# Performance work log

Hardware: AMD Instinct MI355X
Metric: run time of the kernel (lower is better)

## Reference

```python
import jax, jax.numpy as jnp
import numpy as np

Q_MIN = 0.01
PT_THLD = 0.9
MAX_ETA = 4.0
LW_REP = 1.0
LW_NOISE = 0.1
LW_COWARD = 0.1
EPS = 1e-9

N_HITS = 50000
N_CLUSTERS = 1024  # cluster id 0 = noise, ids 1..K-1 = objects
D_EMB = 32


def setup_inputs() -> dict:
    key = jax.random.key(0)
    k0, k1, k2, k3, k4, k5 = jax.random.split(key, 6)
    beta = jax.random.uniform(k0, (N_HITS,), dtype=jnp.float32)
    x = jax.random.normal(k1, (N_HITS, D_EMB), dtype=jnp.float32)
    pt = jax.random.uniform(k2, (N_HITS,), dtype=jnp.float32)
    eta = jax.random.normal(k3, (N_HITS,), dtype=jnp.float32)
    reconstructable = jax.random.randint(k4, (N_HITS,), 0, 2, dtype=jnp.int32)
    cluster_ids = jax.random.randint(k5, (N_HITS,), 0, N_CLUSTERS, dtype=jnp.int64)
    return {
        'beta': beta, 'x': x, 'pt': pt, 'eta': eta,
        'reconstructable': reconstructable, 'cluster_ids': cluster_ids,
        'n_clusters': N_CLUSTERS,
    }


def reference(beta, x, pt, eta, reconstructable, cluster_ids, n_clusters):
    K = int(n_clusters)
    n_hits = beta.shape[0]
    n_part = K - 1  # objects of interest (excluding noise id 0)

    # charge q_j = arctanh(beta)^2 + q_min
    q = jnp.arctanh(jnp.clip(beta, 0.0, 1.0 - 1e-4)) ** 2 + Q_MIN  # [N]

    # attractive membership mask [N, K-1]: hit j belongs to object k and passes filters
    oids = jnp.arange(1, K)
    hit_ok = (reconstructable > 0) & (pt > PT_THLD) & (jnp.abs(eta) < MAX_ETA)
    att = (cluster_ids[:, None] == oids[None, :]) & hit_ok[:, None]
    attf = att.astype(q.dtype)

    # condensation point per object: hit with max charge within the object
    alphas = jnp.argmax(q[:, None] * attf, axis=0)  # [K-1]
    q_k = q[alphas]
    x_k = x[alphas]  # [K-1, D]

    # pairwise Euclidean distances, GEMM form (avoids [N,K,D] intermediate)
    d2 = (jnp.sum(x * x, axis=1)[:, None]
          + jnp.sum(x_k * x_k, axis=1)[None, :]
          - 2.0 * (x @ x_k.T))
    dist = jnp.sqrt(jnp.maximum(d2, 1e-12))  # [N, K-1]

    qw = q[:, None] * q_k[None, :]

    n_hits_oi = jnp.sum(hit_ok).astype(q.dtype)
    norm_att = EPS + n_hits_oi - n_part
    norm_rep = EPS + (n_part - 1) * n_hits

    v_att = jnp.sum(qw * (dist ** 2) * attf) / norm_att

    rep = (~att) & (dist < 1.0)  # max_n_rep=0 -> no subsampling
    v_rep = jnp.sum(qw * (1.0 - dist) * rep.astype(q.dtype)) / norm_rep

    l_coward = jnp.mean(1.0 - beta[alphas])

    noise_mask = (cluster_ids <= 0).astype(q.dtype)  # noise_threshold = 0
    l_noise = jnp.sum(beta * noise_mask) / jnp.maximum(jnp.sum(noise_mask), 1.0)

    total = v_att + LW_REP * v_rep + LW_NOISE * l_noise + LW_COWARD * l_coward
    return total
```

## Files before the change

kernel.cpp:

```cpp
#include <hip/hip_runtime.h>
#include <math.h>

namespace {

constexpr int D = 32;
constexpr int KOBJ = 1023;
constexpr float QMIN = 0.01f;
constexpr float PTT = 0.9f;
constexpr float METAETA = 4.0f;

typedef __attribute__((ext_vector_type(8))) short short8;
typedef __attribute__((ext_vector_type(4))) float f32x4;

#define GLOAD_LDS16(g, l)                                              \
  __builtin_amdgcn_global_load_lds(                                    \
      (const __attribute__((address_space(1))) void*)(g),              \
      (__attribute__((address_space(3))) void*)(l), 16, 0, 0)

__device__ inline float waveSum(float v) {
#pragma unroll
  for (int o = 32; o > 0; o >>= 1) v += __shfl_down(v, o, 64);
  return v;
}

__device__ inline ushort f2bf(float f) {
  unsigned u = __float_as_uint(f);
  return (ushort)((u + 0x7FFFu + ((u >> 16) & 1u)) >> 16);
}

__global__ void k_init(int* wsbase) {
  int i = blockIdx.x * 256 + threadIdx.x;
  if (i < 2064) wsbase[i] = 0;
}

__global__ __launch_bounds__(256) void k_hits(
    const float* __restrict__ beta, const float* __restrict__ x,
    const float* __restrict__ pt, const float* __restrict__ eta,
    const int* __restrict__ recon, const int* __restrict__ cidw,
    int N, float* acc, unsigned long long* keys,
    float* __restrict__ qArr, float* __restrict__ nxArr,
    int* __restrict__ attkArr) {
  int t = threadIdx.x;
  int j = blockIdx.x * 256 + t;
  int odd = 2 * (t & 127) + 1;
  int ow = (odd < N) ? cidw[odd] : 0;
  int is64 = !__any(ow != 0);
  bool ok = false;
  if (j < N) {
    int cid = is64 ? cidw[2 * j] : cidw[j];
    float b = beta[j];
    float bc = fminf(fmaxf(b, 0.f), 1.f - 1e-4f);
    float tt = atanhf(bc);
    float q = tt * tt + QMIN;
    ok = (recon[j] > 0) && (pt[j] > PTT) && (fabsf(eta[j]) < METAETA);
    float nx = 0.f;
    const float4* xr = (const float4*)(x + (size_t)j * D);
#pragma unroll
    for (int i2 = 0; i2 < 8; ++i2) {
      float4 v = xr[i2];
      nx += v.x * v.x + v.y * v.y + v.z * v.z + v.w * v.w;
    }
    int attk = (ok && cid >= 1) ? cid : 0;
    qArr[j] = q;
    nxArr[j] = nx;
    attkArr[j] = attk;
    if (cid <= 0) {
      atomicAdd(&acc[2], b);
      atomicAdd(&acc[3], 1.f);
    }
    if (attk >= 1) {
      unsigned long long key =
          (((unsigned long long)__float_as_uint(q)) << 32) |
          (unsigned long long)(0xFFFFFFFFu - (unsigned)j);
      atomicMax(&keys[attk - 1], key);
    }
  }
  unsigned long long bal = __ballot(ok);
  if ((t & 63) == 0 && bal)
    atomicAdd(&acc[4], (float)__popcll(bal));
}

__global__ __launch_bounds__(256, 2) void k_clusters(
    const float* __restrict__ beta, const float* __restrict__ x,
    const unsigned long long* __restrict__ keys,
    const float* __restrict__ qArr, const float* __restrict__ nxArr,
    int* __restrict__ alphaArr, float2* __restrict__ qnk,
    ushort* __restrict__ xkbT, float* acc) {
  int k = blockIdx.x * blockDim.x + threadIdx.x;
  float cw = 0.f;
  if (k < KOBJ) {
    unsigned long long key = keys[k];
    int alpha = (key != 0ull) ? (int)(0xFFFFFFFFu - (unsigned)(key & 0xFFFFFFFFull)) : 0;
    alphaArr[k] = alpha;
    qnk[k] = make_float2(qArr[alpha], nxArr[alpha]);
    const float4* s4 = (const float4*)(x + (size_t)alpha * D);
    float4 v[8];
#pragma unroll
    for (int i = 0; i < 8; ++i) v[i] = s4[i];
#pragma unroll
    for (int s = 0; s < 4; ++s) {
      float4 v0 = v[2 * s], v1 = v[2 * s + 1];
      ushort* dst = xkbT + (size_t)s * 8192 + (size_t)k * 8;
      dst[0] = f2bf(v0.x); dst[1] = f2bf(v0.y);
      dst[2] = f2bf(v0.z); dst[3] = f2bf(v0.w);
      dst[4] = f2bf(v1.x); dst[5] = f2bf(v1.y);
      dst[6] = f2bf(v1.z); dst[7] = f2bf(v1.w);
    }
    cw = 1.f - beta[alpha];
  } else if (k == KOBJ) {
    qnk[k] = make_float2(0.f, 1e30f);
#pragma unroll
    for (int s = 0; s < 4; ++s) {
      ushort* dst = xkbT + (size_t)s * 8192 + (size_t)k * 8;
#pragma unroll
      for (int e = 0; e < 8; ++e) dst[e] = 0;
    }
  }
  float s = waveSum(cw);
  if ((threadIdx.x & 63) == 0 && s != 0.f) atomicAdd(&acc[5], s);
}

__global__ __launch_bounds__(256) void k_pair(
    const float* __restrict__ x, int N,
    const float* __restrict__ qArr, const float* __restrict__ nxArr,
    const int* __restrict__ attkArr, const int* __restrict__ alphaArr,
    const float2* __restrict__ qnk, const ushort* __restrict__ xkbT,
    float* acc) {
  __shared__ char lds[16384 + 2048 + 64];
  float* redS = (float*)(lds + 18432);
  int t = threadIdx.x;
  int wv = t >> 6;
  int ln = t & 63;
  int ot = blockIdx.y;
  int ob = ot * 256;
  int rowbase = blockIdx.x * 128;

  for (int c = wv; c < 18; c += 4) {
    const char* src;
    if (c < 16)
      src = (const char*)xkbT + (c >> 2) * 16384 + ob * 16 + (c & 3) * 1024;
    else
      src = (const char*)qnk + ob * 8 + (c - 16) * 1024;
    GLOAD_LDS16(src + ln * 16, lds + c * 1024);
  }

  int lr = ln & 15;
  int lk = ln >> 4;
  int wrow = rowbase + wv * 32;

  short8 am2[2];
#pragma unroll
  for (int rt = 0; rt < 2; ++rt) {
    int row = min(wrow + rt * 16 + lr, N - 1);
    const float* p = x + (size_t)row * D + lk * 8;
    float4 v0 = *(const float4*)p;
    float4 v1 = *(const float4*)(p + 4);
    short8 a;
    a[0] = (short)f2bf(-2.f * v0.x); a[1] = (short)f2bf(-2.f * v0.y);
    a[2] = (short)f2bf(-2.f * v0.z); a[3] = (short)f2bf(-2.f * v0.w);
    a[4] = (short)f2bf(-2.f * v1.x); a[5] = (short)f2bf(-2.f * v1.y);
    a[6] = (short)f2bf(-2.f * v1.z); a[7] = (short)f2bf(-2.f * v1.w);
    am2[rt] = a;
  }
  float nxr[2][4], qrow[2][4];
#pragma unroll
  for (int rt = 0; rt < 2; ++rt)
#pragma unroll
    for (int i = 0; i < 4; ++i) {
      int row = wrow + rt * 16 + lk * 4 + i;
      int rc = min(row, N - 1);
      nxr[rt][i] = (row < N) ? nxArr[rc] : 1e37f;
      qrow[rt][i] = (row < N) ? qArr[rc] : 0.f;
    }
  __syncthreads();

  const float2* qnkS = (const float2*)(lds + 16384);
  float rep = 0.f;
#pragma unroll 4
  for (int tt = 0; tt < 16; ++tt) {
    int o = tt * 16 + lr;
    short8 b = *(const short8*)(lds + lk * 4096 + o * 16);
    float2 qn = qnkS[o];
    float nk = qn.y;
    f32x4 c0 = {nxr[0][0] + nk, nxr[0][1] + nk, nxr[0][2] + nk, nxr[0][3] + nk};
    f32x4 c1 = {nxr[1][0] + nk, nxr[1][1] + nk, nxr[1][2] + nk, nxr[1][3] + nk};
    f32x4 s0 = __builtin_amdgcn_mfma_f32_16x16x32_bf16(am2[0], b, c0, 0, 0, 0);
    f32x4 s1 = __builtin_amdgcn_mfma_f32_16x16x32_bf16(am2[1], b, c1, 0, 0, 0);
    float m = fminf(fminf(fminf(s0[0], s0[1]), fminf(s0[2], s0[3])),
                    fminf(fminf(s1[0], s1[1]), fminf(s1[2], s1[3])));
    if (__any(m < 1.f)) {
      float qk = qn.x;
#pragma unroll
      for (int i = 0; i < 4; ++i) {
        if (s0[i] < 1.f)
          rep += qrow[0][i] * qk * (1.f - sqrtf(fmaxf(s0[i], 1e-12f)));
        if (s1[i] < 1.f)
          rep += qrow[1][i] * qk * (1.f - sqrtf(fmaxf(s1[i], 1e-12f)));
      }
    }
  }

  float attc = 0.f, repSub = 0.f;
  if (ot == 0) {
    int j = rowbase + (t >> 1);
    int qt = t & 1;
    if (j < N) {
      int attk = attkArr[j];
      if (attk >= 1) {
        int k0 = attk - 1;
        int alpha = alphaArr[k0];
        float2 qn = qnk[k0];
        const float4* xj = (const float4*)(x + (size_t)j * D + qt * 16);
        const float4* xk = (const float4*)(x + (size_t)alpha * D + qt * 16);
        float dot = 0.f;
#pragma unroll
        for (int i = 0; i < 4; ++i) {
          float4 a = xj[i], bb = xk[i];
          dot += a.x * bb.x + a.y * bb.y + a.z * bb.z + a.w * bb.w;
        }
        dot += __shfl_xor(dot, 1, 2);
        if (qt == 0) {
          float d2 = nxArr[j] + qn.y - 2.f * dot;
          float w = qArr[j] * qn.x;
          attc = w * fmaxf(d2, 1e-12f);
          if (d2 < 1.f)
            repSub = w * (1.f - sqrtf(fmaxf(d2, 1e-12f)));
        }
      }
    }
  }

  float sw = waveSum(rep);
  float sa = waveSum(attc);
  float sr = waveSum(repSub);
  if (ln == 0) {
    redS[wv] = sw;
    redS[4 + wv] = sa;
    redS[8 + wv] = sr;
  }
  __syncthreads();
  if (t == 0) {
    float tot = (redS[0] + redS[1]) + (redS[2] + redS[3]);
    float ta = (redS[4] + redS[5]) + (redS[6] + redS[7]);
    float tr = (redS[8] + redS[9]) + (redS[10] + redS[11]);
    if (tot != tr) atomicAdd(&acc[1], tot - tr);
    if (ta != 0.f) atomicAdd(&acc[0], ta);
  }
}

__global__ void k_final(const float* __restrict__ acc, int N, float* out) {
  if (threadIdx.x == 0 && blockIdx.x == 0) {
    double attSum = acc[0], repSum = acc[1], noiseSum = acc[2];
    double noiseCnt = acc[3], okCnt = acc[4], cowardSum = acc[5];
    double norm_att = 1e-9 + okCnt - (double)KOBJ;
    double norm_rep = 1e-9 + (double)(KOBJ - 1) * (double)N;
    double v_att = attSum / norm_att;
    double v_rep = repSum / norm_rep;
    double l_coward = cowardSum / (double)KOBJ;
    double l_noise = noiseSum / fmax(noiseCnt, 1.0);
    out[0] = (float)(v_att + 1.0 * v_rep + 0.1 * l_noise + 0.1 * l_coward);
  }
}

}

extern "C" void kernel_launch(void* const* d_in, const int* in_sizes, int n_in,
                              void* d_out, int out_size, void* d_ws, size_t ws_size,
                              hipStream_t stream) {
  const float* beta = (const float*)d_in[0];
  const float* x = (const float*)d_in[1];
  const float* pt = (const float*)d_in[2];
  const float* eta = (const float*)d_in[3];
  const int* recon = (const int*)d_in[4];
  const int* cidw = (const int*)d_in[5];
  int N = in_sizes[0];
  float* out = (float*)d_out;

  char* w = (char*)d_ws;
  float* acc = (float*)w;
  unsigned long long* keys = (unsigned long long*)(w + 64);
  int* alphaArr = (int*)(w + 8256);
  float2* qnk = (float2*)(w + 12352);
  ushort* xkbT = (ushort*)(w + 20544);
  float* qArr = (float*)(w + 86080);
  float* nxArr = (float*)(w + 86080 + (size_t)N * 4);
  int* attkArr = (int*)(w + 86080 + (size_t)N * 8);

  int nbN = (N + 255) / 256;
  int rowgroups = (N + 127) / 128;

  k_init<<<9, 256, 0, stream>>>((int*)w);
  k_hits<<<nbN, 256, 0, stream>>>(beta, x, pt, eta, recon, cidw, N,
                                  acc, keys, qArr, nxArr, attkArr);
  k_clusters<<<4, 256, 0, stream>>>(beta, x, keys, qArr, nxArr,
                                    alphaArr, qnk, xkbT, acc);
  dim3 gp(rowgroups, 4);
  k_pair<<<gp, 256, 0, stream>>>(x, N, qArr, nxArr, attkArr,
                                 alphaArr, qnk, xkbT, acc);
  k_final<<<1, 64, 0, stream>>>(acc, N, out);
}
```

Measured before the change: 52.79 us.

## Fuse hit, cluster, pair and final stages into one persistent kernel with grid barriers

Replaces the four stage kernels with a single persistent kernel of 512 blocks. The stages are separated by software grid barriers built on agent-scope atomics, and each stage uses grid-stride loops. The goal is to remove launch overhead and the gaps between dependent kernels. The cluster stage now spreads each object's eight float4 chunks across eight threads. The costs are barrier spin latency, fewer blocks in the pair stage, and a deadlock risk if all 512 blocks cannot be resident at once.

After: 181.4 us. +243.7%, slower.

```diff
diff --git a/kernel.cpp b/kernel.cpp
--- a/kernel.cpp
+++ b/kernel.cpp
@@ -8,6 +8,7 @@
 constexpr float QMIN = 0.01f;
 constexpr float PTT = 0.9f;
 constexpr float METAETA = 4.0f;
+constexpr int NB = 512;
 
 typedef __attribute__((ext_vector_type(8))) short short8;
 typedef __attribute__((ext_vector_type(4))) float f32x4;
@@ -29,227 +30,235 @@
 }
 
 __global__ void k_init(int* wsbase) {
-  int i = blockIdx.x * 256 + threadIdx.x;
-  if (i < 2064) wsbase[i] = 0;
-}
-
-__global__ __launch_bounds__(256) void k_hits(
+  for (int k = threadIdx.x; k < 2064; k += 256) wsbase[k] = 0;
+}
+
+__device__ inline void gridBar(unsigned* bar, int nb, int t, unsigned phase) {
+  __syncthreads();
+  if (t == 0) {
+    unsigned old = __hip_atomic_fetch_add(&bar[0], 1u, __ATOMIC_ACQ_REL,
+                                          __HIP_MEMORY_SCOPE_AGENT);
+    if (old == (unsigned)(nb - 1)) {
+      __hip_atomic_store(&bar[0], 0u, __ATOMIC_RELAXED, __HIP_MEMORY_SCOPE_AGENT);
+      __hip_atomic_fetch_add(&bar[1], 1u, __ATOMIC_ACQ_REL,
+                             __HIP_MEMORY_SCOPE_AGENT);
+    } else {
+      unsigned g;
+      do {
+        __builtin_amdgcn_s_sleep(16);
+        g = __hip_atomic_load(&bar[1], __ATOMIC_RELAXED, __HIP_MEMORY_SCOPE_AGENT);
+      } while (g <= phase);
+      (void)__hip_atomic_load(&bar[1], __ATOMIC_ACQUIRE, __HIP_MEMORY_SCOPE_AGENT);
+    }
+  }
+  __syncthreads();
+}
+
+__global__ __launch_bounds__(256, 4) void k_all(
     const float* __restrict__ beta, const float* __restrict__ x,
     const float* __restrict__ pt, const float* __restrict__ eta,
-    const int* __restrict__ recon, const int* __restrict__ cidw,
-    int N, float* acc, unsigned long long* keys,
-    float* __restrict__ qArr, float* __restrict__ nxArr,
-    int* __restrict__ attkArr) {
-  int t = threadIdx.x;
-  int j = blockIdx.x * 256 + t;
-  int odd = 2 * (t & 127) + 1;
-  int ow = (odd < N) ? cidw[odd] : 0;
-  int is64 = !__any(ow != 0);
-  bool ok = false;
-  if (j < N) {
-    int cid = is64 ? cidw[2 * j] : cidw[j];
-    float b = beta[j];
-    float bc = fminf(fmaxf(b, 0.f), 1.f - 1e-4f);
-    float tt = atanhf(bc);
-    float q = tt * tt + QMIN;
-    ok = (recon[j] > 0) && (pt[j] > PTT) && (fabsf(eta[j]) < METAETA);
-    float nx = 0.f;
-    const float4* xr = (const float4*)(x + (size_t)j * D);
-#pragma unroll
-    for (int i2 = 0; i2 < 8; ++i2) {
-      float4 v = xr[i2];
-      nx += v.x * v.x + v.y * v.y + v.z * v.z + v.w * v.w;
-    }
-    int attk = (ok && cid >= 1) ? cid : 0;
-    qArr[j] = q;
-    nxArr[j] = nx;
-    attkArr[j] = attk;
-    if (cid <= 0) {
-      atomicAdd(&acc[2], b);
-      atomicAdd(&acc[3], 1.f);
-    }
-    if (attk >= 1) {
-      unsigned long long key =
-          (((unsigned long long)__float_as_uint(q)) << 32) |
-          (unsigned long long)(0xFFFFFFFFu - (unsigned)j);
-      atomicMax(&keys[attk - 1], key);
-    }
-  }
-  unsigned long long bal = __ballot(ok);
-  if ((t & 63) == 0 && bal)
-    atomicAdd(&acc[4], (float)__popcll(bal));
-}
-
-__global__ __launch_bounds__(256, 2) void k_clusters(
-    const float* __restrict__ beta, const float* __restrict__ x,
-    const unsigned long long* __restrict__ keys,
-    const float* __restrict__ qArr, const float* __restrict__ nxArr,
+    const int* __restrict__ recon, const int* __restrict__ cidw, int N,
+    float* acc, unsigned* bar, unsigned long long* keys,
     int* __restrict__ alphaArr, float2* __restrict__ qnk,
-    ushort* __restrict__ xkbT, float* acc) {
-  int k = blockIdx.x * blockDim.x + threadIdx.x;
-  float cw = 0.f;
-  if (k < KOBJ) {
-    unsigned long long key = keys[k];
-    int alpha = (key != 0ull) ? (int)(0xFFFFFFFFu - (unsigned)(key & 0xFFFFFFFFull)) : 0;
-    alphaArr[k] = alpha;
-    qnk[k] = make_float2(qArr[alpha], nxArr[alpha]);
-    const float4* s4 = (const float4*)(x + (size_t)alpha * D);
-    float4 v[8];
-#pragma unroll
-    for (int i = 0; i < 8; ++i) v[i] = s4[i];
-#pragma unroll
-    for (int s = 0; s < 4; ++s) {
-      float4 v0 = v[2 * s], v1 = v[2 * s + 1];
-      ushort* dst = xkbT + (size_t)s * 8192 + (size_t)k * 8;
-      dst[0] = f2bf(v0.x); dst[1] = f2bf(v0.y);
-      dst[2] = f2bf(v0.z); dst[3] = f2bf(v0.w);
-      dst[4] = f2bf(v1.x); dst[5] = f2bf(v1.y);
-      dst[6] = f2bf(v1.z); dst[7] = f2bf(v1.w);
-    }
-    cw = 1.f - beta[alpha];
-  } else if (k == KOBJ) {
-    qnk[k] = make_float2(0.f, 1e30f);
-#pragma unroll
-    for (int s = 0; s < 4; ++s) {
-      ushort* dst = xkbT + (size_t)s * 8192 + (size_t)k * 8;
-#pragma unroll
-      for (int e = 0; e < 8; ++e) dst[e] = 0;
-    }
-  }
-  float s = waveSum(cw);
-  if ((threadIdx.x & 63) == 0 && s != 0.f) atomicAdd(&acc[5], s);
-}
-
-__global__ __launch_bounds__(256) void k_pair(
-    const float* __restrict__ x, int N,
-    const float* __restrict__ qArr, const float* __restrict__ nxArr,
-    const int* __restrict__ attkArr, const int* __restrict__ alphaArr,
-    const float2* __restrict__ qnk, const ushort* __restrict__ xkbT,
-    float* acc) {
+    ushort* __restrict__ xkbT, float* __restrict__ qArr,
+    float* __restrict__ nxArr, int* __restrict__ attkArr, float* out) {
   __shared__ char lds[16384 + 2048 + 64];
   float* redS = (float*)(lds + 18432);
-  int t = threadIdx.x;
-  int wv = t >> 6;
-  int ln = t & 63;
-  int ot = blockIdx.y;
-  int ob = ot * 256;
-  int rowbase = blockIdx.x * 128;
-
-  for (int c = wv; c < 18; c += 4) {
-    const char* src;
-    if (c < 16)
-      src = (const char*)xkbT + (c >> 2) * 16384 + ob * 16 + (c & 3) * 1024;
-    else
-      src = (const char*)qnk + ob * 8 + (c - 16) * 1024;
-    GLOAD_LDS16(src + ln * 16, lds + c * 1024);
-  }
-
-  int lr = ln & 15;
-  int lk = ln >> 4;
-  int wrow = rowbase + wv * 32;
-
-  short8 am2[2];
-#pragma unroll
-  for (int rt = 0; rt < 2; ++rt) {
-    int row = min(wrow + rt * 16 + lr, N - 1);
-    const float* p = x + (size_t)row * D + lk * 8;
-    float4 v0 = *(const float4*)p;
-    float4 v1 = *(const float4*)(p + 4);
-    short8 a;
-    a[0] = (short)f2bf(-2.f * v0.x); a[1] = (short)f2bf(-2.f * v0.y);
-    a[2] = (short)f2bf(-2.f * v0.z); a[3] = (short)f2bf(-2.f * v0.w);
-    a[4] = (short)f2bf(-2.f * v1.x); a[5] = (short)f2bf(-2.f * v1.y);
-    a[6] = (short)f2bf(-2.f * v1.z); a[7] = (short)f2bf(-2.f * v1.w);
-    am2[rt] = a;
-  }
-  float nxr[2][4], qrow[2][4];
-#pragma unroll
-  for (int rt = 0; rt < 2; ++rt)
-#pragma unroll
-    for (int i = 0; i < 4; ++i) {
-      int row = wrow + rt * 16 + lk * 4 + i;
-      int rc = min(row, N - 1);
-      nxr[rt][i] = (row < N) ? nxArr[rc] : 1e37f;
-      qrow[rt][i] = (row < N) ? qArr[rc] : 0.f;
-    }
-  __syncthreads();
-
-  const float2* qnkS = (const float2*)(lds + 16384);
-  float rep = 0.f;
+  const int t = threadIdx.x;
+  const int b = blockIdx.x;
+  const int nb = gridDim.x;
+  const int wv = t >> 6;
+  const int ln = t & 63;
+
+  {
+    int odd = 2 * (t & 127) + 1;
+    int ow = (odd < N) ? cidw[odd] : 0;
+    int is64 = !__any(ow != 0);
+    for (int j = b * 256 + t; j < N; j += nb * 256) {
+      int cid = is64 ? cidw[2 * j] : cidw[j];
+      float bv = beta[j];
+      float bc = fminf(fmaxf(bv, 0.f), 1.f - 1e-4f);
+      float th = atanhf(bc);
+      float q = th * th + QMIN;
+      bool ok = (recon[j] > 0) && (pt[j] > PTT) && (fabsf(eta[j]) < METAETA);
+      float nx = 0.f;
+      const float4* xr = (const float4*)(x + (size_t)j * D);
+#pragma unroll
+      for (int i2 = 0; i2 < 8; ++i2) {
+        float4 v = xr[i2];
+        nx += v.x * v.x + v.y * v.y + v.z * v.z + v.w * v.w;
+      }
+      int attk = (ok && cid >= 1) ? cid : 0;
+      qArr[j] = q;
+      nxArr[j] = nx;
+      attkArr[j] = attk;
+      if (cid <= 0) {
+        atomicAdd(&acc[2], bv);
+        atomicAdd(&acc[3], 1.f);
+      }
+      if (attk >= 1) {
+        unsigned long long key =
+            (((unsigned long long)__float_as_uint(q)) << 32) |
+            (unsigned long long)(0xFFFFFFFFu - (unsigned)j);
+        atomicMax(&keys[attk - 1], key);
+      }
+      unsigned long long bal = __ballot(ok);
+      if (ln == 0 && bal) atomicAdd(&acc[4], (float)__popcll(bal));
+    }
+  }
+  gridBar(bar, nb, t, 0);
+
+  {
+    int g = b * 256 + t;
+    int obj = g >> 3, p = g & 7;
+    float cw = 0.f;
+    if (obj <= KOBJ) {
+      if (obj < KOBJ) {
+        unsigned long long key = keys[obj];
+        int alpha = (key != 0ull)
+                        ? (int)(0xFFFFFFFFu - (unsigned)(key & 0xFFFFFFFFull))
+                        : 0;
+        if (p == 0) {
+          alphaArr[obj] = alpha;
+          qnk[obj] = make_float2(qArr[alpha], nxArr[alpha]);
+          cw = 1.f - beta[alpha];
+        }
+        float4 v = *(const float4*)(x + (size_t)alpha * D + p * 4);
+        ushort* dst = xkbT + (size_t)(p >> 1) * 8192 + (size_t)obj * 8 + (p & 1) * 4;
+        dst[0] = f2bf(v.x); dst[1] = f2bf(v.y);
+        dst[2] = f2bf(v.z); dst[3] = f2bf(v.w);
+      } else {
+        if (p == 0) qnk[obj] = make_float2(0.f, 1e30f);
+        ushort* dst = xkbT + (size_t)(p >> 1) * 8192 + (size_t)obj * 8 + (p & 1) * 4;
+        dst[0] = 0; dst[1] = 0; dst[2] = 0; dst[3] = 0;
+      }
+    }
+    float s = waveSum(cw);
+    if (ln == 0 && s != 0.f) atomicAdd(&acc[5], s);
+  }
+  gridBar(bar, nb, t, 1);
+
+  {
+    int ot = b & 3;
+    int ob = ot * 256;
+    for (int c = wv; c < 18; c += 4) {
+      const char* src;
+      if (c < 16)
+        src = (const char*)xkbT + (c >> 2) * 16384 + ob * 16 + (c & 3) * 1024;
+      else
+        src = (const char*)qnk + ob * 8 + (c - 16) * 1024;
+      GLOAD_LDS16(src + ln * 16, lds + c * 1024);
+    }
+    __syncthreads();
+
+    int lr = ln & 15;
+    int lk = ln >> 4;
+    const float2* qnkS = (const float2*)(lds + 16384);
+    float rep = 0.f, attc = 0.f, repSub = 0.f;
+    int rowgroups = (N + 127) / 128;
+
+    for (int rg = b >> 2; rg < rowgroups; rg += nb >> 2) {
+      int rowbase = rg * 128;
+      int wrow = rowbase + wv * 32;
+      short8 am2[2];
+#pragma unroll
+      for (int rt = 0; rt < 2; ++rt) {
+        int row = min(wrow + rt * 16 + lr, N - 1);
+        const float* p = x + (size_t)row * D + lk * 8;
+        float4 v0 = *(const float4*)p;
+        float4 v1 = *(const float4*)(p + 4);
+        short8 a;
+        a[0] = (short)f2bf(-2.f * v0.x); a[1] = (short)f2bf(-2.f * v0.y);
+        a[2] = (short)f2bf(-2.f * v0.z); a[3] = (short)f2bf(-2.f * v0.w);
+        a[4] = (short)f2bf(-2.f * v1.x); a[5] = (short)f2bf(-2.f * v1.y);
+        a[6] = (short)f2bf(-2.f * v1.z); a[7] = (short)f2bf(-2.f * v1.w);
+        am2[rt] = a;
+      }
+      float nxr[2][4], qrow[2][4];
+#pragma unroll
+      for (int rt = 0; rt < 2; ++rt)
+#pragma unroll
+        for (int i = 0; i < 4; ++i) {
+          int row = wrow + rt * 16 + lk * 4 + i;
+          int rc = min(row, N - 1);
+          nxr[rt][i] = (row < N) ? nxArr[rc] : 1e37f;
+          qrow[rt][i] = (row < N) ? qArr[rc] : 0.f;
+        }
+
 #pragma unroll 4
-  for (int tt = 0; tt < 16; ++tt) {
-    int o = tt * 16 + lr;
-    short8 b = *(const short8*)(lds + lk * 4096 + o * 16);
-    float2 qn = qnkS[o];
-    float nk = qn.y;
-    f32x4 c0 = {nxr[0][0] + nk, nxr[0][1] + nk, nxr[0][2] + nk, nxr[0][3] + nk};
-    f32x4 c1 = {nxr[1][0] + nk, nxr[1][1] + nk, nxr[1][2] + nk, nxr[1][3] + nk};
-    f32x4 s0 = __builtin_amdgcn_mfma_f32_16x16x32_bf16(am2[0], b, c0, 0, 0, 0);
-    f32x4 s1 = __builtin_amdgcn_mfma_f32_16x16x32_bf16(am2[1], b, c1, 0, 0, 0);
-    float m = fminf(fminf(fminf(s0[0], s0[1]), fminf(s0[2], s0[3])),
-                    fminf(fminf(s1[0], s1[1]), fminf(s1[2], s1[3])));
-    if (__any(m < 1.f)) {
-      float qk = qn.x;
-#pragma unroll
-      for (int i = 0; i < 4; ++i) {
-        if (s0[i] < 1.f)
-          rep += qrow[0][i] * qk * (1.f - sqrtf(fmaxf(s0[i], 1e-12f)));
-        if (s1[i] < 1.f)
-          rep += qrow[1][i] * qk * (1.f - sqrtf(fmaxf(s1[i], 1e-12f)));
-      }
-    }
-  }
-
-  float attc = 0.f, repSub = 0.f;
-  if (ot == 0) {
-    int j = rowbase + (t >> 1);
-    int qt = t & 1;
-    if (j < N) {
-      int attk = attkArr[j];
-      if (attk >= 1) {
-        int k0 = attk - 1;
-        int alpha = alphaArr[k0];
-        float2 qn = qnk[k0];
-        const float4* xj = (const float4*)(x + (size_t)j * D + qt * 16);
-        const float4* xk = (const float4*)(x + (size_t)alpha * D + qt * 16);
-        float dot = 0.f;
-#pragma unroll
-        for (int i = 0; i < 4; ++i) {
-          float4 a = xj[i], bb = xk[i];
-          dot += a.x * bb.x + a.y * bb.y + a.z * bb.z + a.w * bb.w;
+      for (int tt = 0; tt < 16; ++tt) {
+        int o = tt * 16 + lr;
+        short8 bb = *(const short8*)(lds + lk * 4096 + o * 16);
+        float2 qn = qnkS[o];
+        float nk = qn.y;
+        f32x4 c0 = {nxr[0][0] + nk, nxr[0][1] + nk, nxr[0][2] + nk, nxr[0][3] + nk};
+        f32x4 c1 = {nxr[1][0] + nk, nxr[1][1] + nk, nxr[1][2] + nk, nxr[1][3] + nk};
+        f32x4 s0 = __builtin_amdgcn_mfma_f32_16x16x32_bf16(am2[0], bb, c0, 0, 0, 0);
+        f32x4 s1 = __builtin_amdgcn_mfma_f32_16x16x32_bf16(am2[1], bb, c1, 0, 0, 0);
+        float m = fminf(fminf(fminf(s0[0], s0[1]), fminf(s0[2], s0[3])),
+                        fminf(fminf(s1[0], s1[1]), fminf(s1[2], s1[3])));
+        if (__any(m < 1.f)) {
+          float qk = qn.x;
+#pragma unroll
+          for (int i = 0; i < 4; ++i) {
+            if (s0[i] < 1.f)
+              rep += qrow[0][i] * qk * (1.f - sqrtf(fmaxf(s0[i], 1e-12f)));
+            if (s1[i] < 1.f)
+              rep += qrow[1][i] * qk * (1.f - sqrtf(fmaxf(s1[i], 1e-12f)));
+          }
         }
-        dot += __shfl_xor(dot, 1, 2);
-        if (qt == 0) {
-          float d2 = nxArr[j] + qn.y - 2.f * dot;
-          float w = qArr[j] * qn.x;
-          attc = w * fmaxf(d2, 1e-12f);
-          if (d2 < 1.f)
-            repSub = w * (1.f - sqrtf(fmaxf(d2, 1e-12f)));
+      }
+
+      if (ot == 0) {
+        int j = rowbase + (t >> 1);
+        int qt = t & 1;
+        if (j < N) {
+          int attk = attkArr[j];
+          if (attk >= 1) {
+            int k0 = attk - 1;
+            int alpha = alphaArr[k0];
+            float2 qn = qnk[k0];
+            const float4* xj = (const float4*)(x + (size_t)j * D + qt * 16);
+            const float4* xk = (const float4*)(x + (size_t)alpha * D + qt * 16);
+            float dot = 0.f;
+#pragma unroll
+            for (int i = 0; i < 4; ++i) {
+              float4 a = xj[i], bv = xk[i];
+              dot += a.x * bv.x + a.y * bv.y + a.z * bv.z + a.w * bv.w;
+            }
+            dot += __shfl_xor(dot, 1, 2);
+            if (qt == 0) {
+              float d2 = nxArr[j] + qn.y - 2.f * dot;
+              float w = qArr[j] * qn.x;
+              attc += w * fmaxf(d2, 1e-12f);
+              if (d2 < 1.f)
+                repSub += w * (1.f - sqrtf(fmaxf(d2, 1e-12f)));
+            }
+          }
         }
       }
     }
-  }
-
-  float sw = waveSum(rep);
-  float sa = waveSum(attc);
-  float sr = waveSum(repSub);
-  if (ln == 0) {
-    redS[wv] = sw;
-    redS[4 + wv] = sa;
-    redS[8 + wv] = sr;
-  }
-  __syncthreads();
-  if (t == 0) {
-    float tot = (redS[0] + redS[1]) + (redS[2] + redS[3]);
-    float ta = (redS[4] + redS[5]) + (redS[6] + redS[7]);
-    float tr = (redS[8] + redS[9]) + (redS[10] + redS[11]);
-    if (tot != tr) atomicAdd(&acc[1], tot - tr);
-    if (ta != 0.f) atomicAdd(&acc[0], ta);
-  }
-}
-
-__global__ void k_final(const float* __restrict__ acc, int N, float* out) {
-  if (threadIdx.x == 0 && blockIdx.x == 0) {
+
+    float sw = waveSum(rep);
+    float sa = waveSum(attc);
+    float sr = waveSum(repSub);
+    if (ln == 0) {
+      redS[wv] = sw;
+      redS[4 + wv] = sa;
+      redS[8 + wv] = sr;
+    }
+    __syncthreads();
+    if (t == 0) {
+      float tot = (redS[0] + redS[1]) + (redS[2] + redS[3]);
+      float ta = (redS[4] + redS[5]) + (redS[6] + redS[7]);
+      float tr = (redS[8] + redS[9]) + (redS[10] + redS[11]);
+      if (tot != tr) atomicAdd(&acc[1], tot - tr);
+      if (ta != 0.f) atomicAdd(&acc[0], ta);
+    }
+  }
+  gridBar(bar, nb, t, 2);
+
+  if (b == 0 && t == 0) {
     double attSum = acc[0], repSum = acc[1], noiseSum = acc[2];
     double noiseCnt = acc[3], okCnt = acc[4], cowardSum = acc[5];
     double norm_att = 1e-9 + okCnt - (double)KOBJ;
@@ -278,6 +287,7 @@
 
   char* w = (char*)d_ws;
   float* acc = (float*)w;
+  unsigned* bar = (unsigned*)(w + 32);
   unsigned long long* keys = (unsigned long long*)(w + 64);
   int* alphaArr = (int*)(w + 8256);
   float2* qnk = (float2*)(w + 12352);
@@ -286,16 +296,8 @@
   float* nxArr = (float*)(w + 86080 + (size_t)N * 4);
   int* attkArr = (int*)(w + 86080 + (size_t)N * 8);
 
-  int nbN = (N + 255) / 256;
-  int rowgroups = (N + 127) / 128;
-
-  k_init<<<9, 256, 0, stream>>>((int*)w);
-  k_hits<<<nbN, 256, 0, stream>>>(beta, x, pt, eta, recon, cidw, N,
-                                  acc, keys, qArr, nxArr, attkArr);
-  k_clusters<<<4, 256, 0, stream>>>(beta, x, keys, qArr, nxArr,
-                                    alphaArr, qnk, xkbT, acc);
-  dim3 gp(rowgroups, 4);
-  k_pair<<<gp, 256, 0, stream>>>(x, N, qArr, nxArr, attkArr,
-                                 alphaArr, qnk, xkbT, acc);
-  k_final<<<1, 64, 0, stream>>>(acc, N, out);
-}
+  k_init<<<1, 256, 0, stream>>>((int*)w);
+  k_all<<<NB, 256, 0, stream>>>(beta, x, pt, eta, recon, cidw, N,
+                                acc, bar, keys, alphaArr, qnk, xkbT,
+                                qArr, nxArr, attkArr, out);
+}
```
